# Optimization experiments

Hardware: AMD Instinct MI355X
Metric: run time of the kernel (lower is better)

## Reference

```python
import jax, jax.numpy as jnp
import numpy as np

RING_SIZES = list(range(3, 27, 2))  # 3,5,...,25 -> 12 rings; (1+12)*96 = 1248
BN_EPS = 1e-5


def _box_sum(x, k):
    """Sum over k x k window (k odd), 'same' zero padding. x: [B,C,H,W].
    O(1) per pixel via summed-area table instead of dense depthwise conv."""
    p = k // 2
    H, W = x.shape[2], x.shape[3]
    xp = jnp.pad(x, ((0, 0), (0, 0), (p, p), (p, p)))
    S = jnp.cumsum(jnp.cumsum(xp, axis=2), axis=3)
    S = jnp.pad(S, ((0, 0), (0, 0), (1, 0), (1, 0)))  # leading zero row/col
    return (S[:, :, k:k + H, k:k + W] - S[:, :, :H, k:k + W]
            - S[:, :, k:k + H, :W] + S[:, :, :H, :W])


def _ring_sum(x, k):
    """Depthwise conv with a k x k ring of ones == box(k) - box(k-2)."""
    inner = x if k == 3 else _box_sum(x, k - 2)
    return _box_sum(x, k) - inner


def _bn_eval(x, gamma, beta, mean, var):
    scale = gamma / jnp.sqrt(var + BN_EPS)
    return x * scale[None, :, None, None] + (beta - mean * scale)[None, :, None, None]


def _conv1x1(x, w, b):
    # x: [B,C,H,W], w: [O,C] -> [B,O,H,W]
    return jnp.einsum('bchw,oc->bohw', x, w) + b[None, :, None, None]


def setup_inputs() -> dict:
    key = jax.random.key(0)
    ks = jax.random.split(key, 13)
    B, C, H, W = 4, 96, 128, 128
    return {
        'x': jax.random.normal(ks[0], (B, C, H, W), jnp.float32),
        'bn1_gamma': jax.random.uniform(ks[1], (1248,), jnp.float32, 0.5, 1.5),
        'bn1_beta': jax.random.normal(ks[2], (1248,), jnp.float32) * 0.1,
        'bn1_mean': jax.random.normal(ks[3], (1248,), jnp.float32),
        'bn1_var': jax.random.uniform(ks[4], (1248,), jnp.float32, 0.5, 1.5),
        'conv1_w': jax.random.normal(ks[5], (512, 1248), jnp.float32) * (1.0 / np.sqrt(1248)),
        'conv1_b': jax.random.normal(ks[6], (512,), jnp.float32) * 0.01,
        'bn2_gamma': jax.random.uniform(ks[7], (512,), jnp.float32, 0.5, 1.5),
        'bn2_beta': jax.random.normal(ks[8], (512,), jnp.float32) * 0.1,
        'bn2_mean': jax.random.normal(ks[9], (512,), jnp.float32),
        'bn2_var': jax.random.uniform(ks[10], (512,), jnp.float32, 0.5, 1.5),
        'conv2_w': jax.random.normal(ks[11], (96, 512), jnp.float32) * (1.0 / np.sqrt(512)),
        'conv2_b': jax.random.normal(ks[12], (96,), jnp.float32) * 0.01,
    }


def reference(x, bn1_gamma, bn1_beta, bn1_mean, bn1_var, conv1_w, conv1_b,
              bn2_gamma, bn2_beta, bn2_mean, bn2_var, conv2_w, conv2_b):
    convs = [x] + [_ring_sum(x, k) for k in RING_SIZES]
    h = jnp.concatenate(convs, axis=1)  # [B, 1248, H, W]
    h = _bn_eval(h, bn1_gamma, bn1_beta, bn1_mean, bn1_var)
    h = jax.nn.relu(_conv1x1(h, conv1_w, conv1_b))
    h = _bn_eval(h, bn2_gamma, bn2_beta, bn2_mean, bn2_var)
    return _conv1x1(h, conv2_w, conv2_b)
```

## Files before the change

### kernel.cpp

```cpp
#include <hip/hip_runtime.h>
#include <hip/hip_bf16.h>
#include <cstdint>

typedef __attribute__((ext_vector_type(8))) short bf16x8;
typedef __attribute__((ext_vector_type(4))) short bf16x4;
typedef __attribute__((ext_vector_type(4))) float f32x4;

#define BN_EPS 1e-5f

__device__ __forceinline__ void sat_plane(const float* __restrict__ xp,
                                          float* __restrict__ Sg, int t)
{
  __shared__ float tile[16384];
  __shared__ float csA[512];
  __shared__ float csB[512];

  for (int i4 = t; i4 < 4096; i4 += 512) {
    int r = i4 >> 5;
    int g = i4 & 31;
    float4 v = *(const float4*)(xp + (size_t)r * 128 + g * 4);
    *(float4*)(tile + r * 128 + ((g ^ (r & 31)) << 2)) = v;
  }
  __syncthreads();

  int r = t & 127, ch = t >> 7;
  {
    float carry = 0.f;
#pragma unroll
    for (int g8 = 0; g8 < 8; ++g8) {
      int g = ch * 8 + g8;
      float* p = tile + r * 128 + ((g ^ (r & 31)) << 2);
      float4 v = *(float4*)p;
      float s0 = carry + v.x, s1 = s0 + v.y, s2 = s1 + v.z, s3 = s2 + v.w;
      float4 o; o.x = s0; o.y = s1; o.z = s2; o.w = s3;
      *(float4*)p = o;
      carry = s3;
    }
    csA[r * 4 + ch] = carry;
  }
  __syncthreads();
  if (ch > 0) {
    float offs = csA[r * 4 + 0];
    if (ch > 1) offs += csA[r * 4 + 1];
    if (ch > 2) offs += csA[r * 4 + 2];
#pragma unroll
    for (int g8 = 0; g8 < 8; ++g8) {
      int g = ch * 8 + g8;
      float* p = tile + r * 128 + ((g ^ (r & 31)) << 2);
      float4 v = *(float4*)p;
      v.x += offs; v.y += offs; v.z += offs; v.w += offs;
      *(float4*)p = v;
    }
  }
  __syncthreads();

  int xcol = t & 127, rc = t >> 7;
  int gc = xcol >> 2, wc = xcol & 3;
  float regs[32];
  {
    float run = 0.f;
#pragma unroll
    for (int r8 = 0; r8 < 32; ++r8) {
      int rr = rc * 32 + r8;
      run += tile[rr * 128 + ((gc ^ (rr & 31)) << 2) + wc];
      regs[r8] = run;
    }
    csB[xcol * 4 + rc] = run;
  }
  if (t < 132) Sg[t] = 0.f;
  if (t < 128) Sg[(t + 1) * 132] = 0.f;
  if (t < 128) {
    float* rp = Sg + (size_t)(t + 1) * 132;
    rp[129] = 0.f; rp[130] = 0.f; rp[131] = 0.f;
  }
  __syncthreads();

  float offs = 0.f;
  if (rc > 0) offs += csB[xcol * 4 + 0];
  if (rc > 1) offs += csB[xcol * 4 + 1];
  if (rc > 2) offs += csB[xcol * 4 + 2];
#pragma unroll
  for (int r8 = 0; r8 < 32; ++r8) {
    int rr = rc * 32 + r8;
    Sg[(rr + 1) * 132 + xcol + 1] = regs[r8] + offs;
  }
}

__global__ __launch_bounds__(512) void prepsat_kernel(
    const float* __restrict__ W1, const float* __restrict__ cb1,
    const float* __restrict__ g1, const float* __restrict__ be1,
    const float* __restrict__ mu1, const float* __restrict__ va1,
    const float* __restrict__ W2, const float* __restrict__ cb2,
    const float* __restrict__ g2, const float* __restrict__ be2,
    const float* __restrict__ mu2, const float* __restrict__ va2,
    const float* __restrict__ x,
    __hip_bfloat16* __restrict__ V, float* __restrict__ b1e,
    __hip_bfloat16* __restrict__ W2e, float* __restrict__ b2e,
    float* __restrict__ SAT, int nplanes)
{
  int blk = blockIdx.x;
  int t = threadIdx.x;
  if (blk < 512) {
    __shared__ float red[8];
    int o = blk;
    const float* wrow = W1 + (size_t)o * 1248;
    float acc = 0.f;
    for (int i = t; i < 1248; i += 512) {
      float s = g1[i] * rsqrtf(va1[i] + BN_EPS);
      float w = wrow[i];
      acc += w * (be1[i] - mu1[i] * s);
      float g = w * s;
      float gn = 0.f;
      if (i < 1152) {
        float sn = g1[i + 96] * rsqrtf(va1[i + 96] + BN_EPS);
        gn = wrow[i + 96] * sn;
      }
      V[(size_t)o * 1248 + i] = __float2bfloat16(g - gn);
    }
    for (int d = 32; d > 0; d >>= 1) acc += __shfl_down(acc, d);
    int lane = t & 63, wvv = t >> 6;
    if (lane == 0) red[wvv] = acc;
    __syncthreads();
    if (t == 0) {
      float s = cb1[o];
#pragma unroll
      for (int i = 0; i < 8; ++i) s += red[i];
      b1e[o] = s;
    }
  } else if (blk < 608) {
    __shared__ float red2[8];
    int o = blk - 512;
    const float* wrow = W2 + (size_t)o * 512;
    float acc;
    {
      int j = t;
      float s = g2[j] * rsqrtf(va2[j] + BN_EPS);
      float wv = wrow[j];
      acc = wv * (be2[j] - mu2[j] * s);
      W2e[(size_t)o * 512 + j] = __float2bfloat16(wv * s);
    }
    for (int d = 32; d > 0; d >>= 1) acc += __shfl_down(acc, d);
    int lane = t & 63, wvv = t >> 6;
    if (lane == 0) red2[wvv] = acc;
    __syncthreads();
    if (t == 0) {
      float s = cb2[o];
#pragma unroll
      for (int i = 0; i < 8; ++i) s += red2[i];
      b2e[o] = s;
    }
  } else {
    int plane = blk - 608;
    if (plane < nplanes)
      sat_plane(x + (size_t)plane * 16384, SAT + (size_t)plane * 17028, t);
  }
}

__global__ __launch_bounds__(512) void satonly_kernel(
    const float* __restrict__ x, float* __restrict__ SAT)
{
  sat_plane(x + (size_t)blockIdx.x * 16384,
            SAT + (size_t)blockIdx.x * 17028, threadIdx.x);
}

__global__ __launch_bounds__(512, 2) void fused6_kernel(
    const float* __restrict__ SAT, const __hip_bfloat16* __restrict__ V,
    const float* __restrict__ b1e, const __hip_bfloat16* __restrict__ W2e,
    const float* __restrict__ b2e, float* __restrict__ out, int nb, int b0)
{
  extern __shared__ __align__(16) char smem[];
  float* E0 = (float*)smem;
  float* E1 = (float*)(smem + 50688);
  __hip_bfloat16* As0 = (__hip_bfloat16*)(smem + 101376);
  __hip_bfloat16* As1 = (__hip_bfloat16*)(smem + 129024);

  int blk = blockIdx.x;
  int rows_per_xcd = (nb * 128) >> 3;
  int r = (blk & 7) * rows_per_xcd + (blk >> 3);
  int bL = r >> 7, y = r & 127;

  int t = threadIdx.x;
  int lane = t & 63, wv = t >> 6;
  int wo = wv >> 1, wp = wv & 1;
  int lr = lane & 15, quad = lane >> 4;
  int px = t & 127;
  int bg = t >> 7;

  const float* Sb = SAT + (size_t)bL * 96 * 17028;

  f32x4 acc[8][4];
#pragma unroll
  for (int io = 0; io < 8; ++io)
#pragma unroll
    for (int ip = 0; ip < 4; ++ip) acc[io][ip] = (f32x4){0.f, 0.f, 0.f, 0.f};

  float4 ea[3], eb[3];
  float ta = 0.f, tb = 0.f;

  auto eload = [&](int jr, int h) {
    int y1 = ((y - jr < 0) ? 0 : (y - jr)) * 132;
    int y2 = (((y + jr > 127) ? 127 : (y + jr)) + 1) * 132;
#pragma unroll
    for (int k = 0; k < 3; ++k) {
      int idx = t + 512 * (h * 3 + k);
      int cl = idx >> 5, ck = idx & 31;
      const float* bp = Sb + (size_t)cl * 17028 + ck * 4;
      ea[k] = *(const float4*)(bp + y2);
      eb[k] = *(const float4*)(bp + y1);
    }
    if (h == 1 && t < 96) {
      const float* bp = Sb + (size_t)t * 17028 + 128;
      ta = bp[y2];
      tb = bp[y1];
    }
  };

  auto ewrite = [&](float* E, int h) {
#pragma unroll
    for (int k = 0; k < 3; ++k) {
      int idx = t + 512 * (h * 3 + k);
      int cl = idx >> 5, ck = idx & 31;
      float4 d;
      d.x = ea[k].x - eb[k].x; d.y = ea[k].y - eb[k].y;
      d.z = ea[k].z - eb[k].z; d.w = ea[k].w - eb[k].w;
      *(float4*)(E + cl * 132 + ck * 4) = d;
    }
    if (h == 1 && t < 96) E[t * 132 + 128] = ta - tb;
  };

  auto build_k = [&](const float* E, __hip_bfloat16* As, int jr, int k0, int k1) {
    int x1 = (px - jr < 0) ? 0 : (px - jr);
    int x2 = ((px + jr > 127) ? 127 : (px + jr)) + 1;
#pragma unroll
    for (int k = k0; k < k1; ++k) {
      int g = bg + 4 * k;
      const float* Eb = E + g * 8 * 132;
      union { bf16x8 v; __hip_bfloat16 h8[8]; } pk;
#pragma unroll
      for (int i = 0; i < 8; ++i)
        pk.h8[i] = __float2bfloat16(Eb[i * 132 + x2] - Eb[i * 132 + x1]);
      *(bf16x8*)(As + px * 108 + g * 8) = pk.v;
    }
  };

  auto mfma_sub = [&](int j, int sub, const __hip_bfloat16* As) {
    bf16x8 av[8], bs[4];
#pragma unroll
    for (int io = 0; io < 8; ++io)
      av[io] = *(const bf16x8*)(V + (size_t)(wo * 128 + io * 16 + lr) * 1248
                                + j * 96 + sub * 32 + quad * 8);
#pragma unroll
    for (int ip = 0; ip < 4; ++ip)
      bs[ip] = *(const bf16x8*)(As + (wp * 64 + ip * 16 + lr) * 108 + sub * 32 + quad * 8);
    __builtin_amdgcn_s_setprio(1);
#pragma unroll
    for (int io = 0; io < 8; ++io)
#pragma unroll
      for (int ip = 0; ip < 4; ++ip)
        acc[io][ip] = __builtin_amdgcn_mfma_f32_16x16x32_bf16(av[io], bs[ip], acc[io][ip], 0, 0, 0);
    __builtin_amdgcn_s_setprio(0);
  };

  eload(0, 0); ewrite(E0, 0); eload(0, 1); ewrite(E0, 1);
  __syncthreads();
  eload(1, 0); ewrite(E1, 0);
  build_k(E0, As0, 0, 0, 2);
  eload(1, 1); ewrite(E1, 1);
  build_k(E0, As0, 0, 2, 3);
  __syncthreads();

  for (int j = 0; j < 13; ++j) {
    float* Ew = (j & 1) ? E1 : E0;
    const float* Er = (j & 1) ? E0 : E1;
    const __hip_bfloat16* Asr = (j & 1) ? As1 : As0;
    __hip_bfloat16* Asw = (j & 1) ? As0 : As1;
    bool pf = (j < 11), bd = (j < 12);
    if (pf) eload(j + 2, 0);
    mfma_sub(j, 0, Asr);
    if (pf) ewrite(Ew, 0);
    if (bd) build_k(Er, Asw, j + 1, 0, 2);
    if (pf) eload(j + 2, 1);
    mfma_sub(j, 1, Asr);
    if (pf) ewrite(Ew, 1);
    if (bd) build_k(Er, Asw, j + 1, 2, 3);
    mfma_sub(j, 2, Asr);
    __syncthreads();
  }

  __hip_bfloat16* Yst = (__hip_bfloat16*)smem;
#pragma unroll
  for (int io = 0; io < 8; ++io) {
    int o1b = wo * 128 + io * 16 + quad * 4;
    float4 bias = *(const float4*)(b1e + o1b);
#pragma unroll
    for (int ip = 0; ip < 4; ++ip) {
      int pxx = wp * 64 + ip * 16 + lr;
      f32x4 a = acc[io][ip];
      float z0 = a[0] + bias.x; z0 = z0 > 0.f ? z0 : 0.f;
      float z1 = a[1] + bias.y; z1 = z1 > 0.f ? z1 : 0.f;
      float z2 = a[2] + bias.z; z2 = z2 > 0.f ? z2 : 0.f;
      float z3 = a[3] + bias.w; z3 = z3 > 0.f ? z3 : 0.f;
      union { bf16x4 v; __hip_bfloat16 hh[4]; } pk;
      pk.hh[0] = __float2bfloat16(z0); pk.hh[1] = __float2bfloat16(z1);
      pk.hh[2] = __float2bfloat16(z2); pk.hh[3] = __float2bfloat16(z3);
      *(bf16x4*)(Yst + pxx * 520 + o1b) = pk.v;
    }
  }
  __syncthreads();

  int og = wv >> 2;
  int pg = wv & 3;
  f32x4 acc2[3][2];
#pragma unroll
  for (int im = 0; im < 3; ++im)
#pragma unroll
    for (int tl = 0; tl < 2; ++tl) acc2[im][tl] = (f32x4){0.f, 0.f, 0.f, 0.f};

  for (int k2 = 0; k2 < 512; k2 += 32) {
    bf16x8 bfr2[2];
#pragma unroll
    for (int tl = 0; tl < 2; ++tl)
      bfr2[tl] = *(const bf16x8*)(Yst + (pg * 32 + tl * 16 + lr) * 520 + k2 + quad * 8);
#pragma unroll
    for (int im = 0; im < 3; ++im) {
      bf16x8 afr2 = *(const bf16x8*)(W2e + (size_t)(og * 48 + im * 16 + lr) * 512
                                     + k2 + quad * 8);
#pragma unroll
      for (int tl = 0; tl < 2; ++tl)
        acc2[im][tl] = __builtin_amdgcn_mfma_f32_16x16x32_bf16(afr2, bfr2[tl], acc2[im][tl], 0, 0, 0);
    }
  }

  size_t obase = ((size_t)(b0 + bL) * 96) * 16384 + (size_t)y * 128;
#pragma unroll
  for (int im = 0; im < 3; ++im) {
#pragma unroll
    for (int tl = 0; tl < 2; ++tl) {
      int pxx = pg * 32 + tl * 16 + lr;
#pragma unroll
      for (int rr = 0; rr < 4; ++rr) {
        int o2 = og * 48 + im * 16 + quad * 4 + rr;
        out[obase + (size_t)o2 * 16384 + pxx] = acc2[im][tl][rr] + b2e[o2];
      }
    }
  }
}

extern "C" void kernel_launch(void* const* d_in, const int* in_sizes, int n_in,
                              void* d_out, int out_size, void* d_ws, size_t ws_size,
                              hipStream_t stream)
{
  const float* x   = (const float*)d_in[0];
  const float* g1  = (const float*)d_in[1];
  const float* be1 = (const float*)d_in[2];
  const float* mu1 = (const float*)d_in[3];
  const float* va1 = (const float*)d_in[4];
  const float* W1  = (const float*)d_in[5];
  const float* cb1 = (const float*)d_in[6];
  const float* g2  = (const float*)d_in[7];
  const float* be2 = (const float*)d_in[8];
  const float* mu2 = (const float*)d_in[9];
  const float* va2 = (const float*)d_in[10];
  const float* W2  = (const float*)d_in[11];
  const float* cb2 = (const float*)d_in[12];
  float* out = (float*)d_out;

  hipFuncSetAttribute((const void*)fused6_kernel,
                      hipFuncAttributeMaxDynamicSharedMemorySize, 156672);

  char* w = (char*)d_ws;
  __hip_bfloat16* V   = (__hip_bfloat16*)w; w += (size_t)512 * 1248 * 2;
  __hip_bfloat16* W2e = (__hip_bfloat16*)w; w += (size_t)96 * 512 * 2;
  float* b1e = (float*)w; w += 2048;
  float* b2e = (float*)w; w += 512;
  size_t fixed = (size_t)(w - (char*)d_ws);

  const size_t satB = (size_t)96 * 17028 * 4;
  int nb = (ws_size >= fixed + 4 * satB + 4096) ? 4 : 1;

  float* SAT = (float*)w;

  if (nb == 4) {
    prepsat_kernel<<<992, 512, 0, stream>>>(W1, cb1, g1, be1, mu1, va1,
                                            W2, cb2, g2, be2, mu2, va2,
                                            x, V, b1e, W2e, b2e, SAT, 384);
    fused6_kernel<<<512, 512, 156672, stream>>>(SAT, V, b1e, W2e, b2e, out, 4, 0);
  } else {
    prepsat_kernel<<<608, 512, 0, stream>>>(W1, cb1, g1, be1, mu1, va1,
                                            W2, cb2, g2, be2, mu2, va2,
                                            x, V, b1e, W2e, b2e, SAT, 0);
    for (int b0 = 0; b0 < 4; ++b0) {
      satonly_kernel<<<96, 512, 0, stream>>>(x + (size_t)b0 * 96 * 16384, SAT);
      fused6_kernel<<<128, 512, 156672, stream>>>(SAT, V, b1e, W2e, b2e, out, 1, b0);
    }
  }
}
```

Before: 283.4 us.

## Replace 2D SAT with row prefix sums and split output channels across blocks

The prep stage now writes only row-wise prefix sums per plane instead of a full 2D summed-area table. The fused kernel accumulates column strips in shared memory incrementally, adding rows y±jr at each ring step, and drops the double-buffered E/As staging. Each block now computes half of the 512 hidden channels, with twice as many blocks, half the shared memory and a target of 4 blocks per CU. Partial second-GEMM results are combined with atomicAdd into an output that is zeroed by memset first. This adds atomic traffic, a memset and more syncs per step, and removes pipelining overlap.

After: 623.3 us. +120.0%, slower.

```diff
diff --git a/kernel.cpp b/kernel.cpp
--- a/kernel.cpp
+++ b/kernel.cpp
@@ -7,13 +7,13 @@
 typedef __attribute__((ext_vector_type(4))) float f32x4;
 
 #define BN_EPS 1e-5f
-
-__device__ __forceinline__ void sat_plane(const float* __restrict__ xp,
-                                          float* __restrict__ Sg, int t)
+#define PROWS 16896
+
+__device__ __forceinline__ void prow_plane(const float* __restrict__ xp,
+                                           float* __restrict__ Pg, int t)
 {
   __shared__ float tile[16384];
   __shared__ float csA[512];
-  __shared__ float csB[512];
 
   for (int i4 = t; i4 < 4096; i4 += 512) {
     int r = i4 >> 5;
@@ -52,37 +52,18 @@
       *(float4*)p = v;
     }
   }
+  if (t < 128) {
+    float* rp = Pg + (size_t)t * 132;
+    rp[0] = 0.f; rp[129] = 0.f; rp[130] = 0.f; rp[131] = 0.f;
+  }
   __syncthreads();
 
   int xcol = t & 127, rc = t >> 7;
   int gc = xcol >> 2, wc = xcol & 3;
-  float regs[32];
-  {
-    float run = 0.f;
-#pragma unroll
-    for (int r8 = 0; r8 < 32; ++r8) {
-      int rr = rc * 32 + r8;
-      run += tile[rr * 128 + ((gc ^ (rr & 31)) << 2) + wc];
-      regs[r8] = run;
-    }
-    csB[xcol * 4 + rc] = run;
-  }
-  if (t < 132) Sg[t] = 0.f;
-  if (t < 128) Sg[(t + 1) * 132] = 0.f;
-  if (t < 128) {
-    float* rp = Sg + (size_t)(t + 1) * 132;
-    rp[129] = 0.f; rp[130] = 0.f; rp[131] = 0.f;
-  }
-  __syncthreads();
-
-  float offs = 0.f;
-  if (rc > 0) offs += csB[xcol * 4 + 0];
-  if (rc > 1) offs += csB[xcol * 4 + 1];
-  if (rc > 2) offs += csB[xcol * 4 + 2];
 #pragma unroll
   for (int r8 = 0; r8 < 32; ++r8) {
     int rr = rc * 32 + r8;
-    Sg[(rr + 1) * 132 + xcol + 1] = regs[r8] + offs;
+    Pg[rr * 132 + xcol + 1] = tile[rr * 128 + ((gc ^ (rr & 31)) << 2) + wc];
   }
 }
 
@@ -96,7 +77,7 @@
     const float* __restrict__ x,
     __hip_bfloat16* __restrict__ V, float* __restrict__ b1e,
     __hip_bfloat16* __restrict__ W2e, float* __restrict__ b2e,
-    float* __restrict__ SAT, int nplanes)
+    float* __restrict__ P, int nplanes)
 {
   int blk = blockIdx.x;
   int t = threadIdx.x;
@@ -152,87 +133,109 @@
   } else {
     int plane = blk - 608;
     if (plane < nplanes)
-      sat_plane(x + (size_t)plane * 16384, SAT + (size_t)plane * 17028, t);
+      prow_plane(x + (size_t)plane * 16384, P + (size_t)plane * PROWS, t);
   }
 }
 
-__global__ __launch_bounds__(512) void satonly_kernel(
-    const float* __restrict__ x, float* __restrict__ SAT)
+__global__ __launch_bounds__(512) void prowonly_kernel(
+    const float* __restrict__ x, float* __restrict__ P)
 {
-  sat_plane(x + (size_t)blockIdx.x * 16384,
-            SAT + (size_t)blockIdx.x * 17028, threadIdx.x);
+  prow_plane(x + (size_t)blockIdx.x * 16384,
+             P + (size_t)blockIdx.x * PROWS, threadIdx.x);
 }
 
-__global__ __launch_bounds__(512, 2) void fused6_kernel(
-    const float* __restrict__ SAT, const __hip_bfloat16* __restrict__ V,
+__global__ __launch_bounds__(512, 4) void fused7_kernel(
+    const float* __restrict__ P, const __hip_bfloat16* __restrict__ V,
     const float* __restrict__ b1e, const __hip_bfloat16* __restrict__ W2e,
     const float* __restrict__ b2e, float* __restrict__ out, int nb, int b0)
 {
   extern __shared__ __align__(16) char smem[];
-  float* E0 = (float*)smem;
-  float* E1 = (float*)(smem + 50688);
-  __hip_bfloat16* As0 = (__hip_bfloat16*)(smem + 101376);
-  __hip_bfloat16* As1 = (__hip_bfloat16*)(smem + 129024);
-
-  int blk = blockIdx.x;
-  int rows_per_xcd = (nb * 128) >> 3;
-  int r = (blk & 7) * rows_per_xcd + (blk >> 3);
-  int bL = r >> 7, y = r & 127;
+  float* E = (float*)smem;
+  __hip_bfloat16* As = (__hip_bfloat16*)(smem + 50688);
+
+  int b = blockIdx.x;
+  int rows = nb * 128, per_xcd = rows >> 3;
+  int xcd = b & 7, rest = b >> 3;
+  int mh = rest & 1;
+  int ridx = xcd * per_xcd + (rest >> 1);
+  int bL = ridx >> 7, y = ridx & 127;
 
   int t = threadIdx.x;
   int lane = t & 63, wv = t >> 6;
-  int wo = wv >> 1, wp = wv & 1;
+  int wm = wv & 3, wn = wv >> 2;
   int lr = lane & 15, quad = lane >> 4;
   int px = t & 127;
   int bg = t >> 7;
 
-  const float* Sb = SAT + (size_t)bL * 96 * 17028;
-
-  f32x4 acc[8][4];
-#pragma unroll
-  for (int io = 0; io < 8; ++io)
+  const float* Pb = P + (size_t)bL * 96 * PROWS;
+
+  f32x4 acc[4][4];
+#pragma unroll
+  for (int io = 0; io < 4; ++io)
 #pragma unroll
     for (int ip = 0; ip < 4; ++ip) acc[io][ip] = (f32x4){0.f, 0.f, 0.f, 0.f};
 
-  float4 ea[3], eb[3];
-  float ta = 0.f, tb = 0.f;
-
-  auto eload = [&](int jr, int h) {
-    int y1 = ((y - jr < 0) ? 0 : (y - jr)) * 132;
-    int y2 = (((y + jr > 127) ? 127 : (y + jr)) + 1) * 132;
+  float4 pa[3], pb[3];
+
+  auto el = [&](int jr, int s0, int n) {
+    int ra = y + jr, rb = y - jr;
+    bool fa = (ra <= 127), fb = (rb >= 0);
 #pragma unroll
     for (int k = 0; k < 3; ++k) {
-      int idx = t + 512 * (h * 3 + k);
-      int cl = idx >> 5, ck = idx & 31;
-      const float* bp = Sb + (size_t)cl * 17028 + ck * 4;
-      ea[k] = *(const float4*)(bp + y2);
-      eb[k] = *(const float4*)(bp + y1);
-    }
-    if (h == 1 && t < 96) {
-      const float* bp = Sb + (size_t)t * 17028 + 128;
-      ta = bp[y2];
-      tb = bp[y1];
+      if (k >= n) break;
+      int idx = (s0 + k) * 512 + t;
+      if (idx < 3168) {
+        int cl = idx / 33, ck = idx - cl * 33;
+        const float* gp = Pb + (size_t)cl * PROWS + ck * 4;
+        if (fa) pa[k] = *(const float4*)(gp + ra * 132);
+        if (fb) pb[k] = *(const float4*)(gp + rb * 132);
+      }
     }
   };
 
-  auto ewrite = [&](float* E, int h) {
+  auto ermw = [&](int jr, int s0, int n) {
+    bool fa = (y + jr <= 127), fb = (y - jr >= 0);
 #pragma unroll
     for (int k = 0; k < 3; ++k) {
-      int idx = t + 512 * (h * 3 + k);
-      int cl = idx >> 5, ck = idx & 31;
-      float4 d;
-      d.x = ea[k].x - eb[k].x; d.y = ea[k].y - eb[k].y;
-      d.z = ea[k].z - eb[k].z; d.w = ea[k].w - eb[k].w;
-      *(float4*)(E + cl * 132 + ck * 4) = d;
-    }
-    if (h == 1 && t < 96) E[t * 132 + 128] = ta - tb;
+      if (k >= n) break;
+      int idx = (s0 + k) * 512 + t;
+      if (idx < 3168) {
+        int cl = idx / 33, ck = idx - cl * 33;
+        float* ep = E + cl * 132 + ck * 4;
+        float4 v = *(float4*)ep;
+        if (fa) { v.x += pa[k].x; v.y += pa[k].y; v.z += pa[k].z; v.w += pa[k].w; }
+        if (fb) { v.x += pb[k].x; v.y += pb[k].y; v.z += pb[k].z; v.w += pb[k].w; }
+        *(float4*)ep = v;
+      }
+    }
   };
 
-  auto build_k = [&](const float* E, __hip_bfloat16* As, int jr, int k0, int k1) {
+  auto einit = [&](int s0, int n) {
+#pragma unroll
+    for (int k = 0; k < 3; ++k) {
+      if (k >= n) break;
+      int idx = (s0 + k) * 512 + t;
+      if (idx < 3168) {
+        int cl = idx / 33, ck = idx - cl * 33;
+        pa[k] = *(const float4*)(Pb + (size_t)cl * PROWS + y * 132 + ck * 4);
+      }
+    }
+#pragma unroll
+    for (int k = 0; k < 3; ++k) {
+      if (k >= n) break;
+      int idx = (s0 + k) * 512 + t;
+      if (idx < 3168) {
+        int cl = idx / 33, ck = idx - cl * 33;
+        *(float4*)(E + cl * 132 + ck * 4) = pa[k];
+      }
+    }
+  };
+
+  auto build = [&](int jr) {
     int x1 = (px - jr < 0) ? 0 : (px - jr);
     int x2 = ((px + jr > 127) ? 127 : (px + jr)) + 1;
 #pragma unroll
-    for (int k = k0; k < k1; ++k) {
+    for (int k = 0; k < 3; ++k) {
       int g = bg + 4 * k;
       const float* Eb = E + g * 8 * 132;
       union { bf16x8 v; __hip_bfloat16 h8[8]; } pk;
@@ -243,58 +246,55 @@
     }
   };
 
-  auto mfma_sub = [&](int j, int sub, const __hip_bfloat16* As) {
-    bf16x8 av[8], bs[4];
-#pragma unroll
-    for (int io = 0; io < 8; ++io)
-      av[io] = *(const bf16x8*)(V + (size_t)(wo * 128 + io * 16 + lr) * 1248
+  auto mfma_sub = [&](int j, int sub) {
+    bf16x8 av[4], bs[4];
+#pragma unroll
+    for (int io = 0; io < 4; ++io)
+      av[io] = *(const bf16x8*)(V + (size_t)(mh * 256 + wm * 64 + io * 16 + lr) * 1248
                                 + j * 96 + sub * 32 + quad * 8);
 #pragma unroll
     for (int ip = 0; ip < 4; ++ip)
-      bs[ip] = *(const bf16x8*)(As + (wp * 64 + ip * 16 + lr) * 108 + sub * 32 + quad * 8);
+      bs[ip] = *(const bf16x8*)(As + (wn * 64 + ip * 16 + lr) * 108 + sub * 32 + quad * 8);
     __builtin_amdgcn_s_setprio(1);
 #pragma unroll
-    for (int io = 0; io < 8; ++io)
+    for (int io = 0; io < 4; ++io)
 #pragma unroll
       for (int ip = 0; ip < 4; ++ip)
-        acc[io][ip] = __builtin_amdgcn_mfma_f32_16x16x32_bf16(av[io], bs[ip], acc[io][ip], 0, 0, 0);
+        acc[io][ip] = __builtin_amdgcn_mfma_f32_16x16x32_bf16(
+            av[io], bs[ip], acc[io][ip], 0, 0, 0);
     __builtin_amdgcn_s_setprio(0);
   };
 
-  eload(0, 0); ewrite(E0, 0); eload(0, 1); ewrite(E0, 1);
-  __syncthreads();
-  eload(1, 0); ewrite(E1, 0);
-  build_k(E0, As0, 0, 0, 2);
-  eload(1, 1); ewrite(E1, 1);
-  build_k(E0, As0, 0, 2, 3);
+  einit(0, 3); einit(3, 3); einit(6, 1);
+  __syncthreads();
+  build(0);
   __syncthreads();
 
   for (int j = 0; j < 13; ++j) {
-    float* Ew = (j & 1) ? E1 : E0;
-    const float* Er = (j & 1) ? E0 : E1;
-    const __hip_bfloat16* Asr = (j & 1) ? As1 : As0;
-    __hip_bfloat16* Asw = (j & 1) ? As0 : As1;
-    bool pf = (j < 11), bd = (j < 12);
-    if (pf) eload(j + 2, 0);
-    mfma_sub(j, 0, Asr);
-    if (pf) ewrite(Ew, 0);
-    if (bd) build_k(Er, Asw, j + 1, 0, 2);
-    if (pf) eload(j + 2, 1);
-    mfma_sub(j, 1, Asr);
-    if (pf) ewrite(Ew, 1);
-    if (bd) build_k(Er, Asw, j + 1, 2, 3);
-    mfma_sub(j, 2, Asr);
+    int jr = j + 1;
+    bool up = (j < 12);
+    if (up) el(jr, 0, 2);
+    mfma_sub(j, 0);
+    if (up) { ermw(jr, 0, 2); el(jr, 2, 2); }
+    mfma_sub(j, 1);
+    if (up) { ermw(jr, 2, 2); el(jr, 4, 3); }
+    mfma_sub(j, 2);
+    if (up) ermw(jr, 4, 3);
     __syncthreads();
+    if (up) {
+      build(jr);
+      __syncthreads();
+    }
   }
 
   __hip_bfloat16* Yst = (__hip_bfloat16*)smem;
 #pragma unroll
-  for (int io = 0; io < 8; ++io) {
-    int o1b = wo * 128 + io * 16 + quad * 4;
-    float4 bias = *(const float4*)(b1e + o1b);
+  for (int io = 0; io < 4; ++io) {
+    int o1b = wm * 64 + io * 16 + quad * 4;
+    float4 bias = *(const float4*)(b1e + mh * 256 + o1b);
 #pragma unroll
     for (int ip = 0; ip < 4; ++ip) {
-      int pxx = wp * 64 + ip * 16 + lr;
+      int pxx = wn * 64 + ip * 16 + lr;
       f32x4 a = acc[io][ip];
       float z0 = a[0] + bias.x; z0 = z0 > 0.f ? z0 : 0.f;
       float z1 = a[1] + bias.y; z1 = z1 > 0.f ? z1 : 0.f;
@@ -303,7 +303,7 @@
       union { bf16x4 v; __hip_bfloat16 hh[4]; } pk;
       pk.hh[0] = __float2bfloat16(z0); pk.hh[1] = __float2bfloat16(z1);
       pk.hh[2] = __float2bfloat16(z2); pk.hh[3] = __float2bfloat16(z3);
-      *(bf16x4*)(Yst + pxx * 520 + o1b) = pk.v;
+      *(bf16x4*)(Yst + pxx * 264 + o1b) = pk.v;
     }
   }
   __syncthreads();
@@ -316,15 +316,15 @@
 #pragma unroll
     for (int tl = 0; tl < 2; ++tl) acc2[im][tl] = (f32x4){0.f, 0.f, 0.f, 0.f};
 
-  for (int k2 = 0; k2 < 512; k2 += 32) {
+  for (int k2 = 0; k2 < 256; k2 += 32) {
     bf16x8 bfr2[2];
 #pragma unroll
     for (int tl = 0; tl < 2; ++tl)
-      bfr2[tl] = *(const bf16x8*)(Yst + (pg * 32 + tl * 16 + lr) * 520 + k2 + quad * 8);
+      bfr2[tl] = *(const bf16x8*)(Yst + (pg * 32 + tl * 16 + lr) * 264 + k2 + quad * 8);
 #pragma unroll
     for (int im = 0; im < 3; ++im) {
       bf16x8 afr2 = *(const bf16x8*)(W2e + (size_t)(og * 48 + im * 16 + lr) * 512
-                                     + k2 + quad * 8);
+                                     + mh * 256 + k2 + quad * 8);
 #pragma unroll
       for (int tl = 0; tl < 2; ++tl)
         acc2[im][tl] = __builtin_amdgcn_mfma_f32_16x16x32_bf16(afr2, bfr2[tl], acc2[im][tl], 0, 0, 0);
@@ -340,7 +340,8 @@
 #pragma unroll
       for (int rr = 0; rr < 4; ++rr) {
         int o2 = og * 48 + im * 16 + quad * 4 + rr;
-        out[obase + (size_t)o2 * 16384 + pxx] = acc2[im][tl][rr] + b2e[o2];
+        float v = acc2[im][tl][rr] + (mh == 0 ? b2e[o2] : 0.f);
+        atomicAdd(&out[obase + (size_t)o2 * 16384 + pxx], v);
       }
     }
   }
@@ -365,8 +366,8 @@
   const float* cb2 = (const float*)d_in[12];
   float* out = (float*)d_out;
 
-  hipFuncSetAttribute((const void*)fused6_kernel,
-                      hipFuncAttributeMaxDynamicSharedMemorySize, 156672);
+  hipFuncSetAttribute((const void*)fused7_kernel,
+                      hipFuncAttributeMaxDynamicSharedMemorySize, 78336);
 
   char* w = (char*)d_ws;
   __hip_bfloat16* V   = (__hip_bfloat16*)w; w += (size_t)512 * 1248 * 2;
@@ -375,23 +376,25 @@
   float* b2e = (float*)w; w += 512;
   size_t fixed = (size_t)(w - (char*)d_ws);
 
-  const size_t satB = (size_t)96 * 17028 * 4;
-  int nb = (ws_size >= fixed + 4 * satB + 4096) ? 4 : 1;
-
-  float* SAT = (float*)w;
+  const size_t pB = (size_t)96 * PROWS * 4;
+  int nb = (ws_size >= fixed + 4 * pB + 4096) ? 4 : 1;
+
+  float* P = (float*)w;
+
+  hipMemsetAsync(out, 0, (size_t)out_size * sizeof(float), stream);
 
   if (nb == 4) {
     prepsat_kernel<<<992, 512, 0, stream>>>(W1, cb1, g1, be1, mu1, va1,
                                             W2, cb2, g2, be2, mu2, va2,
-                                            x, V, b1e, W2e, b2e, SAT, 384);
-    fused6_kernel<<<512, 512, 156672, stream>>>(SAT, V, b1e, W2e, b2e, out, 4, 0);
+                                            x, V, b1e, W2e, b2e, P, 384);
+    fused7_kernel<<<1024, 512, 78336, stream>>>(P, V, b1e, W2e, b2e, out, 4, 0);
   } else {
     prepsat_kernel<<<608, 512, 0, stream>>>(W1, cb1, g1, be1, mu1, va1,
                                             W2, cb2, g2, be2, mu2, va2,
-                                            x, V, b1e, W2e, b2e, SAT, 0);
+                                            x, V, b1e, W2e, b2e, P, 0);
     for (int b0 = 0; b0 < 4; ++b0) {
-      satonly_kernel<<<96, 512, 0, stream>>>(x + (size_t)b0 * 96 * 16384, SAT);
-      fused6_kernel<<<128, 512, 156672, stream>>>(SAT, V, b1e, W2e, b2e, out, 1, b0);
+      prowonly_kernel<<<96, 512, 0, stream>>>(x + (size_t)b0 * 96 * 16384, P);
+      fused7_kernel<<<256, 512, 78336, stream>>>(P, V, b1e, W2e, b2e, out, 1, b0);
     }
   }
 }
```

## Switch first GEMM to 32x32x16 MFMA with register-prefetched weight fragments

Applied to the files above, without the earlier changes.

Replaces the 16x16x32 bf16 MFMA tiling of the conv1 GEMM with 32x32x16 MFMA tiles (4x2 per wave) and reworks the epilogue to match the new accumulator layout. Weight fragments from global memory are now double-buffered in registers and loaded one k-step ahead, so their latency overlaps the MFMAs. The larger tiles cut fragment loads per FLOP and instruction count. The cost is more accumulator registers plus the prefetch buffers, which adds register pressure under the 2-blocks-per-CU launch bound.

Measured after the change: 298.5 us. +5.3%, slower.

```diff
diff --git a/kernel.cpp b/kernel.cpp
--- a/kernel.cpp
+++ b/kernel.cpp
@@ -5,6 +5,7 @@
 typedef __attribute__((ext_vector_type(8))) short bf16x8;
 typedef __attribute__((ext_vector_type(4))) short bf16x4;
 typedef __attribute__((ext_vector_type(4))) float f32x4;
+typedef __attribute__((ext_vector_type(16))) float f32x16;
 
 #define BN_EPS 1e-5f
 
@@ -163,7 +164,7 @@
             SAT + (size_t)blockIdx.x * 17028, threadIdx.x);
 }
 
-__global__ __launch_bounds__(512, 2) void fused6_kernel(
+__global__ __launch_bounds__(512, 2) void fused8_kernel(
     const float* __restrict__ SAT, const __hip_bfloat16* __restrict__ V,
     const float* __restrict__ b1e, const __hip_bfloat16* __restrict__ W2e,
     const float* __restrict__ b2e, float* __restrict__ out, int nb, int b0)
@@ -183,16 +184,20 @@
   int lane = t & 63, wv = t >> 6;
   int wo = wv >> 1, wp = wv & 1;
   int lr = lane & 15, quad = lane >> 4;
+  int cl = lane & 31, kh = lane >> 5;
   int px = t & 127;
   int bg = t >> 7;
 
   const float* Sb = SAT + (size_t)bL * 96 * 17028;
-
-  f32x4 acc[8][4];
-#pragma unroll
-  for (int io = 0; io < 8; ++io)
-#pragma unroll
-    for (int ip = 0; ip < 4; ++ip) acc[io][ip] = (f32x4){0.f, 0.f, 0.f, 0.f};
+  const __hip_bfloat16* Vbase = V + (size_t)(wo * 128 + cl) * 1248 + kh * 8;
+
+  f32x16 acc[4][2];
+#pragma unroll
+  for (int mt = 0; mt < 4; ++mt)
+#pragma unroll
+    for (int nt = 0; nt < 2; ++nt)
+#pragma unroll
+      for (int e = 0; e < 16; ++e) acc[mt][nt][e] = 0.f;
 
   float4 ea[3], eb[3];
   float ta = 0.f, tb = 0.f;
@@ -203,8 +208,8 @@
 #pragma unroll
     for (int k = 0; k < 3; ++k) {
       int idx = t + 512 * (h * 3 + k);
-      int cl = idx >> 5, ck = idx & 31;
-      const float* bp = Sb + (size_t)cl * 17028 + ck * 4;
+      int cc = idx >> 5, ck = idx & 31;
+      const float* bp = Sb + (size_t)cc * 17028 + ck * 4;
       ea[k] = *(const float4*)(bp + y2);
       eb[k] = *(const float4*)(bp + y1);
     }
@@ -219,11 +224,11 @@
 #pragma unroll
     for (int k = 0; k < 3; ++k) {
       int idx = t + 512 * (h * 3 + k);
-      int cl = idx >> 5, ck = idx & 31;
+      int cc = idx >> 5, ck = idx & 31;
       float4 d;
       d.x = ea[k].x - eb[k].x; d.y = ea[k].y - eb[k].y;
       d.z = ea[k].z - eb[k].z; d.w = ea[k].w - eb[k].w;
-      *(float4*)(E + cl * 132 + ck * 4) = d;
+      *(float4*)(E + cc * 132 + ck * 4) = d;
     }
     if (h == 1 && t < 96) E[t * 132 + 128] = ta - tb;
   };
@@ -243,23 +248,31 @@
     }
   };
 
-  auto mfma_sub = [&](int j, int sub, const __hip_bfloat16* As) {
-    bf16x8 av[8], bs[4];
-#pragma unroll
-    for (int io = 0; io < 8; ++io)
-      av[io] = *(const bf16x8*)(V + (size_t)(wo * 128 + io * 16 + lr) * 1248
-                                + j * 96 + sub * 32 + quad * 8);
-#pragma unroll
-    for (int ip = 0; ip < 4; ++ip)
-      bs[ip] = *(const bf16x8*)(As + (wp * 64 + ip * 16 + lr) * 108 + sub * 32 + quad * 8);
+  auto ldV = [&](bf16x8 (&dst)[4], int j, int ks) {
+    const __hip_bfloat16* p = Vbase + j * 96 + ks * 16;
+#pragma unroll
+    for (int mt = 0; mt < 4; ++mt)
+      dst[mt] = *(const bf16x8*)(p + (size_t)mt * 32 * 1248);
+  };
+
+  auto step = [&](bf16x8 (&cur)[4], bf16x8 (&nxt)[4], int pj, int pk, bool pf,
+                  const __hip_bfloat16* As, int ks) {
+    if (pf) ldV(nxt, pj, pk);
+    bf16x8 bs[2];
+#pragma unroll
+    for (int nt = 0; nt < 2; ++nt)
+      bs[nt] = *(const bf16x8*)(As + (wp * 64 + nt * 32 + cl) * 108 + ks * 16 + kh * 8);
     __builtin_amdgcn_s_setprio(1);
 #pragma unroll
-    for (int io = 0; io < 8; ++io)
-#pragma unroll
-      for (int ip = 0; ip < 4; ++ip)
-        acc[io][ip] = __builtin_amdgcn_mfma_f32_16x16x32_bf16(av[io], bs[ip], acc[io][ip], 0, 0, 0);
+    for (int mt = 0; mt < 4; ++mt)
+#pragma unroll
+      for (int nt = 0; nt < 2; ++nt)
+        acc[mt][nt] = __builtin_amdgcn_mfma_f32_32x32x16_bf16(
+            cur[mt], bs[nt], acc[mt][nt], 0, 0, 0);
     __builtin_amdgcn_s_setprio(0);
   };
+
+  bf16x8 av0[4], av1[4];
 
   eload(0, 0); ewrite(E0, 0); eload(0, 1); ewrite(E0, 1);
   __syncthreads();
@@ -267,6 +280,7 @@
   build_k(E0, As0, 0, 0, 2);
   eload(1, 1); ewrite(E1, 1);
   build_k(E0, As0, 0, 2, 3);
+  ldV(av0, 0, 0);
   __syncthreads();
 
   for (int j = 0; j < 13; ++j) {
@@ -275,35 +289,42 @@
     const __hip_bfloat16* Asr = (j & 1) ? As1 : As0;
     __hip_bfloat16* Asw = (j & 1) ? As0 : As1;
     bool pf = (j < 11), bd = (j < 12);
+
     if (pf) eload(j + 2, 0);
-    mfma_sub(j, 0, Asr);
+    step(av0, av1, j, 1, true, Asr, 0);
+    step(av1, av0, j, 2, true, Asr, 1);
     if (pf) ewrite(Ew, 0);
     if (bd) build_k(Er, Asw, j + 1, 0, 2);
     if (pf) eload(j + 2, 1);
-    mfma_sub(j, 1, Asr);
+    step(av0, av1, j, 3, true, Asr, 2);
+    step(av1, av0, j, 4, true, Asr, 3);
     if (pf) ewrite(Ew, 1);
     if (bd) build_k(Er, Asw, j + 1, 2, 3);
-    mfma_sub(j, 2, Asr);
+    step(av0, av1, j, 5, true, Asr, 4);
+    step(av1, av0, j + 1, 0, j < 12, Asr, 5);
     __syncthreads();
   }
 
   __hip_bfloat16* Yst = (__hip_bfloat16*)smem;
 #pragma unroll
-  for (int io = 0; io < 8; ++io) {
-    int o1b = wo * 128 + io * 16 + quad * 4;
-    float4 bias = *(const float4*)(b1e + o1b);
-#pragma unroll
-    for (int ip = 0; ip < 4; ++ip) {
-      int pxx = wp * 64 + ip * 16 + lr;
-      f32x4 a = acc[io][ip];
-      float z0 = a[0] + bias.x; z0 = z0 > 0.f ? z0 : 0.f;
-      float z1 = a[1] + bias.y; z1 = z1 > 0.f ? z1 : 0.f;
-      float z2 = a[2] + bias.z; z2 = z2 > 0.f ? z2 : 0.f;
-      float z3 = a[3] + bias.w; z3 = z3 > 0.f ? z3 : 0.f;
-      union { bf16x4 v; __hip_bfloat16 hh[4]; } pk;
-      pk.hh[0] = __float2bfloat16(z0); pk.hh[1] = __float2bfloat16(z1);
-      pk.hh[2] = __float2bfloat16(z2); pk.hh[3] = __float2bfloat16(z3);
-      *(bf16x4*)(Yst + pxx * 520 + o1b) = pk.v;
+  for (int mt = 0; mt < 4; ++mt) {
+#pragma unroll
+    for (int q = 0; q < 4; ++q) {
+      int o1b = wo * 128 + mt * 32 + q * 8 + kh * 4;
+      float4 bias = *(const float4*)(b1e + o1b);
+#pragma unroll
+      for (int nt = 0; nt < 2; ++nt) {
+        int pxx = wp * 64 + nt * 32 + cl;
+        f32x16 a = acc[mt][nt];
+        float z0 = a[q * 4 + 0] + bias.x; z0 = z0 > 0.f ? z0 : 0.f;
+        float z1 = a[q * 4 + 1] + bias.y; z1 = z1 > 0.f ? z1 : 0.f;
+        float z2 = a[q * 4 + 2] + bias.z; z2 = z2 > 0.f ? z2 : 0.f;
+        float z3 = a[q * 4 + 3] + bias.w; z3 = z3 > 0.f ? z3 : 0.f;
+        union { bf16x4 v; __hip_bfloat16 hh[4]; } pk;
+        pk.hh[0] = __float2bfloat16(z0); pk.hh[1] = __float2bfloat16(z1);
+        pk.hh[2] = __float2bfloat16(z2); pk.hh[3] = __float2bfloat16(z3);
+        *(bf16x4*)(Yst + pxx * 520 + o1b) = pk.v;
+      }
     }
   }
   __syncthreads();
@@ -365,7 +386,7 @@
   const float* cb2 = (const float*)d_in[12];
   float* out = (float*)d_out;
 
-  hipFuncSetAttribute((const void*)fused6_kernel,
+  hipFuncSetAttribute((const void*)fused8_kernel,
                       hipFuncAttributeMaxDynamicSharedMemorySize, 156672);
 
   char* w = (char*)d_ws;
@@ -384,14 +405,14 @@
     prepsat_kernel<<<992, 512, 0, stream>>>(W1, cb1, g1, be1, mu1, va1,
                                             W2, cb2, g2, be2, mu2, va2,
                                             x, V, b1e, W2e, b2e, SAT, 384);
-    fused6_kernel<<<512, 512, 156672, stream>>>(SAT, V, b1e, W2e, b2e, out, 4, 0);
+    fused8_kernel<<<512, 512, 156672, stream>>>(SAT, V, b1e, W2e, b2e, out, 4, 0);
   } else {
     prepsat_kernel<<<608, 512, 0, stream>>>(W1, cb1, g1, be1, mu1, va1,
                                             W2, cb2, g2, be2, mu2, va2,
                                             x, V, b1e, W2e, b2e, SAT, 0);
     for (int b0 = 0; b0 < 4; ++b0) {
       satonly_kernel<<<96, 512, 0, stream>>>(x + (size_t)b0 * 96 * 16384, SAT);
-      fused6_kernel<<<128, 512, 156672, stream>>>(SAT, V, b1e, W2e, b2e, out, 1, b0);
+      fused8_kernel<<<128, 512, 156672, stream>>>(SAT, V, b1e, W2e, b2e, out, 1, b0);
     }
   }
 }
```
